# Performance work log

Hardware: AMD Instinct MI355X
Metric: run time of the kernel (lower is better)

## Reference

```python
import jax, jax.numpy as jnp
import numpy as np

NOISE_DIM = 32
HIDDEN_DIM = 256
DATA_DIM = 2
TEMP = 0.05
N = 16384
DIAG_PENALTY = 1e6


def _cdist(a, b):
    # Euclidean pairwise distance [Na, Nb], safe sqrt (zero grad at d==0 like torch.cdist)
    d2 = (jnp.sum(a * a, -1)[:, None] + jnp.sum(b * b, -1)[None, :]
          - 2.0 * (a @ b.T))
    d2 = jnp.maximum(d2, 0.0)
    safe = jnp.where(d2 > 0, d2, 1.0)
    return jnp.where(d2 > 0, jnp.sqrt(safe), 0.0)


def setup_inputs() -> dict:
    key = jax.random.key(0)
    ks = jax.random.split(key, 12)
    pos = jax.random.normal(ks[0], (N, DATA_DIM), dtype=jnp.float32)
    z = jax.random.normal(ks[1], (N, NOISE_DIM), dtype=jnp.float32)
    def lin(k, fan_in, fan_out):
        bound = 1.0 / np.sqrt(fan_in)
        k1, k2 = jax.random.split(k)
        W = jax.random.uniform(k1, (fan_in, fan_out), minval=-bound, maxval=bound, dtype=jnp.float32)
        b = jax.random.uniform(k2, (fan_out,), minval=-bound, maxval=bound, dtype=jnp.float32)
        return W, b
    W1, b1 = lin(ks[2], NOISE_DIM, HIDDEN_DIM)
    W2, b2 = lin(ks[3], HIDDEN_DIM, HIDDEN_DIM)
    W3, b3 = lin(ks[4], HIDDEN_DIM, HIDDEN_DIM)
    W4, b4 = lin(ks[5], HIDDEN_DIM, HIDDEN_DIM)
    W5, b5 = lin(ks[6], HIDDEN_DIM, DATA_DIM)
    return {"pos": pos, "z": z, "W1": W1, "b1": b1, "W2": W2, "b2": b2,
            "W3": W3, "b3": b3, "W4": W4, "b4": b4, "W5": W5, "b5": b5}


def reference(pos, z, W1, b1, W2, b2, W3, b3, W4, b4, W5, b5):
    # SELU MLP generator
    h = jax.nn.selu(z @ W1 + b1)
    h = jax.nn.selu(h @ W2 + b2)
    h = jax.nn.selu(h @ W3 + b3)
    h = jax.nn.selu(h @ W4 + b4)
    gen = h @ W5 + b5  # [N, D]

    y_pos = jax.lax.stop_gradient(pos)
    y_neg = jax.lax.stop_gradient(gen)

    dist_pos = _cdist(gen, y_pos)  # [N, N]
    dist_neg = _cdist(gen, y_neg)  # [N, N]
    dist_neg = dist_neg + jnp.eye(gen.shape[0], dtype=gen.dtype) * DIAG_PENALTY

    energy_pos = -TEMP * jax.nn.logsumexp(-dist_pos / TEMP, axis=1)
    energy_neg = TEMP * jax.nn.logsumexp(-dist_neg / TEMP, axis=1)
    return energy_pos + energy_neg  # [N]
```

## Files before the change

kernel.cpp:

```cpp
#include <hip/hip_runtime.h>
#include <hip/hip_bf16.h>

#define N_PTS 16384
#define TEMP_F 0.05f

typedef __attribute__((ext_vector_type(8))) short bf16x8;
typedef __attribute__((ext_vector_type(4))) float f32x4;

__device__ __forceinline__ float selu_f(float x) {
    const float scale = 1.0507009873554805f;
    const float alpha = 1.6732632423543772f;
    return x > 0.f ? scale * x : scale * alpha * (__expf(x) - 1.f);
}

__device__ __forceinline__ float fast_sqrtf(float x) {
#if __has_builtin(__builtin_amdgcn_sqrtf)
    return __builtin_amdgcn_sqrtf(x);
#else
    return sqrtf(x);
#endif
}

__device__ __forceinline__ float fast_exp2f(float x) {
#if __has_builtin(__builtin_amdgcn_exp2f)
    return __builtin_amdgcn_exp2f(x);
#else
    return exp2f(x);
#endif
}

__device__ __forceinline__ float fast_log2f(float x) {
#if __has_builtin(__builtin_amdgcn_logf)
    return __builtin_amdgcn_logf(x);
#else
    return log2f(x);
#endif
}

__device__ __forceinline__ f32x4 mfma_bf16(bf16x8 a, bf16x8 b, f32x4 c) {
    return __builtin_amdgcn_mfma_f32_16x16x32_bf16(a, b, c, 0, 0, 0);
}

__device__ __forceinline__ void split_bf16(float v, unsigned short& hi, unsigned short& lo) {
    unsigned u = __float_as_uint(v);
    hi = (unsigned short)(u >> 16);
    float ah = __uint_as_float(u & 0xFFFF0000u);
    lo = (unsigned short)(__float_as_uint(v - ah) >> 16);
}

__global__ __launch_bounds__(256) void pack_kernel(
    const float* __restrict__ W1, const float* __restrict__ W2,
    const float* __restrict__ W3, const float* __restrict__ W4,
    unsigned short* __restrict__ pk)
{
    int idx = blockIdx.x * 256 + threadIdx.x;
    if (idx >= 25600) return;
    const float* src;
    unsigned short *dh, *dl;
    int nt, kc, l, KC;
    if (idx < 1024) {
        src = W1; dh = pk; dl = pk + 8192; KC = 1;
        nt = idx >> 6; kc = 0; l = idx & 63;
    } else {
        int t2 = idx - 1024;
        int ly = t2 >> 13;
        int r2 = t2 & 8191;
        src = (ly == 0) ? W2 : (ly == 1) ? W3 : W4;
        dh = pk + 16384 + ly * 131072;
        dl = dh + 65536;
        KC = 8;
        nt = r2 >> 9; kc = (r2 >> 6) & 7; l = r2 & 63;
    }
    int lr = l & 15, lq = l >> 4;
    int n = nt * 16 + lr;
    bf16x8 hv, lv;
    #pragma unroll
    for (int e = 0; e < 8; e++) {
        int k = kc * 32 + lq * 8 + e;
        float v = src[k * 256 + n];
        unsigned short hb, lb;
        split_bf16(v, hb, lb);
        hv[e] = (short)hb; lv[e] = (short)lb;
    }
    int base = ((nt * KC + kc) * 64 + l) * 8;
    *(bf16x8*)(dh + base) = hv;
    *(bf16x8*)(dl + base) = lv;
}

__global__ __launch_bounds__(512) void mlp_mfma_kernel(
    const float* __restrict__ z,
    const unsigned short* __restrict__ pk,
    const float* __restrict__ b1, const float* __restrict__ b2,
    const float* __restrict__ b3, const float* __restrict__ b4,
    const float* __restrict__ W5, const float* __restrict__ b5,
    float* __restrict__ gen)
{
    __shared__ __align__(16) unsigned short Hh[32 * 256];
    __shared__ __align__(16) unsigned short Hl[32 * 256];

    const int t  = threadIdx.x;
    const int l  = t & 63;
    const int wv = t >> 6;
    const int lr = l & 15;
    const int lq = l >> 4;
    const int row0 = blockIdx.x * 32;

    f32x4 acc[2][2];

    {
        bf16x8 ah[2], al[2];
        #pragma unroll
        for (int m = 0; m < 2; m++) {
            const float* zp = z + (row0 + m * 16 + lr) * 32 + lq * 8;
            f32x4 z0 = *(const f32x4*)(zp);
            f32x4 z1 = *(const f32x4*)(zp + 4);
            #pragma unroll
            for (int e = 0; e < 8; e++) {
                float v = (e < 4) ? z0[e] : z1[e - 4];
                unsigned short hb, lb;
                split_bf16(v, hb, lb);
                ah[m][e] = (short)hb; al[m][e] = (short)lb;
            }
        }
        #pragma unroll
        for (int n2 = 0; n2 < 2; n2++) {
            float bv = b1[wv * 32 + n2 * 16 + lr];
            #pragma unroll
            for (int m = 0; m < 2; m++) acc[m][n2] = (f32x4){bv, bv, bv, bv};
        }
        const bf16x8* B1h = (const bf16x8*)(pk);
        const bf16x8* B1l = (const bf16x8*)(pk + 8192);
        #pragma unroll
        for (int n2 = 0; n2 < 2; n2++) {
            int nt = wv * 2 + n2;
            bf16x8 bh = B1h[nt * 64 + l];
            bf16x8 bl = B1l[nt * 64 + l];
            #pragma unroll
            for (int m = 0; m < 2; m++) {
                acc[m][n2] = mfma_bf16(ah[m], bh, acc[m][n2]);
                acc[m][n2] = mfma_bf16(ah[m], bl, acc[m][n2]);
                acc[m][n2] = mfma_bf16(al[m], bh, acc[m][n2]);
            }
        }
        #pragma unroll
        for (int m = 0; m < 2; m++) {
            #pragma unroll
            for (int n2 = 0; n2 < 2; n2++) {
                #pragma unroll
                for (int r = 0; r < 4; r++) {
                    float v = selu_f(acc[m][n2][r]);
                    int rowo = m * 16 + lq * 4 + r;
                    int n = wv * 32 + n2 * 16 + lr;
                    int o = (2 * n) ^ ((rowo & 7) << 4);
                    unsigned short hb, lb;
                    split_bf16(v, hb, lb);
                    Hh[rowo * 256 + (o >> 1)] = hb;
                    Hl[rowo * 256 + (o >> 1)] = lb;
                }
            }
        }
    }
    __syncthreads();

    #pragma unroll 1
    for (int ly = 0; ly < 3; ly++) {
        const unsigned short* wbase = pk + 16384 + ly * 131072;
        const bf16x8* Bh = (const bf16x8*)(wbase);
        const bf16x8* Bl = (const bf16x8*)(wbase + 65536);
        const float* bb = (ly == 0) ? b2 : (ly == 1) ? b3 : b4;
        #pragma unroll
        for (int n2 = 0; n2 < 2; n2++) {
            float bv = bb[wv * 32 + n2 * 16 + lr];
            #pragma unroll
            for (int m = 0; m < 2; m++) acc[m][n2] = (f32x4){bv, bv, bv, bv};
        }
        #pragma unroll 4
        for (int kc = 0; kc < 8; kc++) {
            bf16x8 ah[2], al[2];
            #pragma unroll
            for (int m = 0; m < 2; m++) {
                int arow = m * 16 + lr;
                int o = (kc * 64 + lq * 16) ^ ((arow & 7) << 4);
                ah[m] = *(const bf16x8*)(Hh + arow * 256 + (o >> 1));
                al[m] = *(const bf16x8*)(Hl + arow * 256 + (o >> 1));
            }
            #pragma unroll
            for (int n2 = 0; n2 < 2; n2++) {
                bf16x8 bh = Bh[((wv * 2 + n2) * 8 + kc) * 64 + l];
                bf16x8 bl = Bl[((wv * 2 + n2) * 8 + kc) * 64 + l];
                #pragma unroll
                for (int m = 0; m < 2; m++) {
                    acc[m][n2] = mfma_bf16(ah[m], bh, acc[m][n2]);
                    acc[m][n2] = mfma_bf16(ah[m], bl, acc[m][n2]);
                    acc[m][n2] = mfma_bf16(al[m], bh, acc[m][n2]);
                }
            }
        }
        __syncthreads();
        #pragma unroll
        for (int m = 0; m < 2; m++) {
            #pragma unroll
            for (int n2 = 0; n2 < 2; n2++) {
                #pragma unroll
                for (int r = 0; r < 4; r++) {
                    float v = selu_f(acc[m][n2][r]);
                    int rowo = m * 16 + lq * 4 + r;
                    int n = wv * 32 + n2 * 16 + lr;
                    int o = (2 * n) ^ ((rowo & 7) << 4);
                    unsigned short hb, lb;
                    split_bf16(v, hb, lb);
                    Hh[rowo * 256 + (o >> 1)] = hb;
                    Hl[rowo * 256 + (o >> 1)] = lb;
                }
            }
        }
        __syncthreads();
    }

    if (t < 64) {
        int row = t & 31;
        int d = t >> 5;
        float sum = b5[d];
        #pragma unroll 4
        for (int k = 0; k < 256; k += 8) {
            int o = (2 * k) ^ ((row & 7) << 4);
            bf16x8 hh = *(const bf16x8*)(Hh + row * 256 + (o >> 1));
            bf16x8 ll = *(const bf16x8*)(Hl + row * 256 + (o >> 1));
            #pragma unroll
            for (int e = 0; e < 8; e++) {
                float hv = __uint_as_float(((unsigned)(unsigned short)hh[e]) << 16)
                         + __uint_as_float(((unsigned)(unsigned short)ll[e]) << 16);
                sum = fmaf(hv, W5[(k + e) * 2 + d], sum);
            }
        }
        gen[(row0 + row) * 2 + d] = sum;
    }
}

__global__ __launch_bounds__(1024) void mlp_kernel(
    const float* __restrict__ z,
    const float* __restrict__ W1, const float* __restrict__ b1,
    const float* __restrict__ W2, const float* __restrict__ b2,
    const float* __restrict__ W3, const float* __restrict__ b3,
    const float* __restrict__ W4, const float* __restrict__ b4,
    const float* __restrict__ W5, const float* __restrict__ b5,
    float* __restrict__ gen)
{
    __shared__ float h[256 * 64];

    const int t = threadIdx.x;
    const int r = t & 63;
    const int w = __builtin_amdgcn_readfirstlane(t >> 6);
    const int c0 = w * 16;
    const int row0 = blockIdx.x * 64;

    #pragma unroll
    for (int e = 0; e < 2; e++) {
        int f  = t + e * 1024;
        int rz = f >> 5;
        int kz = f & 31;
        h[kz * 64 + rz] = z[(row0 + rz) * 32 + kz];
    }
    __syncthreads();

    float acc[16];

    #pragma unroll
    for (int j = 0; j < 16; j++) acc[j] = b1[c0 + j];
    #pragma unroll 8
    for (int k = 0; k < 32; k++) {
        float hv = h[k * 64 + r];
        const float* Wr = W1 + k * 256 + c0;
        #pragma unroll
        for (int j = 0; j < 16; j++) acc[j] = fmaf(hv, Wr[j], acc[j]);
    }
    __syncthreads();
    #pragma unroll
    for (int j = 0; j < 16; j++) h[(c0 + j) * 64 + r] = selu_f(acc[j]);
    __syncthreads();

    for (int layer = 0; layer < 3; layer++) {
        const float* W = (layer == 0) ? W2 : (layer == 1) ? W3 : W4;
        const float* b = (layer == 0) ? b2 : (layer == 1) ? b3 : b4;
        #pragma unroll
        for (int j = 0; j < 16; j++) acc[j] = b[c0 + j];
        #pragma unroll 4
        for (int k = 0; k < 256; k++) {
            float hv = h[k * 64 + r];
            const float* Wr = W + k * 256 + c0;
            #pragma unroll
            for (int j = 0; j < 16; j++) acc[j] = fmaf(hv, Wr[j], acc[j]);
        }
        __syncthreads();
        #pragma unroll
        for (int j = 0; j < 16; j++) h[(c0 + j) * 64 + r] = selu_f(acc[j]);
        __syncthreads();
    }

    float p0 = 0.f, p1 = 0.f;
    #pragma unroll
    for (int kk = 0; kk < 16; kk++) {
        int k = c0 + kk;
        float hv = h[k * 64 + r];
        p0 = fmaf(hv, W5[k * 2 + 0], p0);
        p1 = fmaf(hv, W5[k * 2 + 1], p1);
    }
    __syncthreads();
    h[(0 * 16 + w) * 64 + r] = p0;
    h[(1 * 16 + w) * 64 + r] = p1;
    __syncthreads();
    if (t < 128) {
        int d  = t >> 6;
        int rr = t & 63;
        float sum = b5[d];
        #pragma unroll
        for (int ss = 0; ss < 16; ss++) sum += h[(d * 16 + ss) * 64 + rr];
        gen[(row0 + rr) * 2 + d] = sum;
    }
}

__global__ __launch_bounds__(512) void energy_kernel(
    const float* __restrict__ gen,
    const float* __restrict__ pos,
    float* __restrict__ out,
    int row_off)
{
    __shared__ float4 sp[512];
    __shared__ float4 sg[512];

    const int t  = threadIdx.x;
    const int s  = t & 31;
    const int rl = t >> 5;
    const int i  = row_off + blockIdx.x * 16 + rl;
    const int diagBase = ((row_off + blockIdx.x * 16) >> 10) << 10;

    const float2 q = ((const float2*)gen)[i];

    const float cL2 = 28.853900817779268f;
    const float Tl2 = 0.034657359027997264f;
    const float cB  = 57.707801635558536f;

    float p0 = 0.f, p1 = 0.f, n0 = 0.f, n1 = 0.f;

    for (int base = 0; base < N_PTS; base += 1024) {
        __syncthreads();
        sp[t] = ((const float4*)pos)[base / 2 + t];
        sg[t] = ((const float4*)gen)[base / 2 + t];
        __syncthreads();
        if (base == diagBase) {
            #pragma unroll 4
            for (int u = 0; u < 16; u++) {
                int j = base + 2 * (s + 32 * u);
                float4 pp = sp[s + 32 * u];
                float4 gg = sg[s + 32 * u];
                float dx = q.x - pp.x, dy = q.y - pp.y;
                float d  = fast_sqrtf(fmaf(dx, dx, dy * dy));
                p0 += fast_exp2f(fmaf(-cL2, d, cB));
                dx = q.x - pp.z; dy = q.y - pp.w;
                d  = fast_sqrtf(fmaf(dx, dx, dy * dy));
                p1 += fast_exp2f(fmaf(-cL2, d, cB));
                dx = q.x - gg.x; dy = q.y - gg.y;
                d  = fast_sqrtf(fmaf(dx, dx, dy * dy));
                float e0 = fast_exp2f(fmaf(-cL2, d, cB));
                n0 += (j == i) ? 0.f : e0;
                dx = q.x - gg.z; dy = q.y - gg.w;
                d  = fast_sqrtf(fmaf(dx, dx, dy * dy));
                float e1 = fast_exp2f(fmaf(-cL2, d, cB));
                n1 += (j + 1 == i) ? 0.f : e1;
            }
        } else {
            #pragma unroll 4
            for (int u = 0; u < 16; u++) {
                float4 pp = sp[s + 32 * u];
                float4 gg = sg[s + 32 * u];
                float dx = q.x - pp.x, dy = q.y - pp.y;
                float d  = fast_sqrtf(fmaf(dx, dx, dy * dy));
                p0 += fast_exp2f(fmaf(-cL2, d, cB));
                dx = q.x - pp.z; dy = q.y - pp.w;
                d  = fast_sqrtf(fmaf(dx, dx, dy * dy));
                p1 += fast_exp2f(fmaf(-cL2, d, cB));
                dx = q.x - gg.x; dy = q.y - gg.y;
                d  = fast_sqrtf(fmaf(dx, dx, dy * dy));
                n0 += fast_exp2f(fmaf(-cL2, d, cB));
                dx = q.x - gg.z; dy = q.y - gg.w;
                d  = fast_sqrtf(fmaf(dx, dx, dy * dy));
                n1 += fast_exp2f(fmaf(-cL2, d, cB));
            }
        }
    }

    float sump = p0 + p1;
    float sumn = n0 + n1;
    #pragma unroll
    for (int m = 1; m < 32; m <<= 1) {
        sump += __shfl_xor(sump, m, 32);
        sumn += __shfl_xor(sumn, m, 32);
    }

    if (s == 0) {
        out[i] = Tl2 * (fast_log2f(sumn) - fast_log2f(sump));
    }
}

extern "C" void kernel_launch(void* const* d_in, const int* in_sizes, int n_in,
                              void* d_out, int out_size, void* d_ws, size_t ws_size,
                              hipStream_t stream) {
    const float* pos = (const float*)d_in[0];
    const float* z   = (const float*)d_in[1];
    const float* W1  = (const float*)d_in[2];
    const float* b1  = (const float*)d_in[3];
    const float* W2  = (const float*)d_in[4];
    const float* b2  = (const float*)d_in[5];
    const float* W3  = (const float*)d_in[6];
    const float* b3  = (const float*)d_in[7];
    const float* W4  = (const float*)d_in[8];
    const float* b4  = (const float*)d_in[9];
    const float* W5  = (const float*)d_in[10];
    const float* b5  = (const float*)d_in[11];

    float* gen = (float*)d_ws;
    unsigned short* pk = (unsigned short*)((char*)d_ws + 131072);
    const size_t WS_NEEDED = 131072 + (size_t)409600 * 2;

    if (ws_size >= WS_NEEDED) {
        pack_kernel<<<100, 256, 0, stream>>>(W1, W2, W3, W4, pk);
        mlp_mfma_kernel<<<N_PTS / 32, 512, 0, stream>>>(z, pk, b1, b2, b3, b4,
                                                        W5, b5, gen);
    } else {
        mlp_kernel<<<N_PTS / 64, 1024, 0, stream>>>(z, W1, b1, W2, b2, W3, b3,
                                                    W4, b4, W5, b5, gen);
    }
    energy_kernel<<<N_PTS / 32, 512, 0, stream>>>(gen, pos, (float*)d_out, 0);
    energy_kernel<<<N_PTS / 32, 512, 0, stream>>>(gen, pos, (float*)d_out, 8192);
}
```

Measured before the change: 249.0 us.

## Fuse weight packing, MLP and energy into one cooperative kernel

Replaces the four separate launches (pack, MLP, two energy halves) with a single cooperative kernel of 512 blocks that uses grid-wide syncs between the weight-packing, MLP and pairwise-energy phases. Each block handles 32 MLP rows and then 2x16 energy rows. The intent is to remove launch overhead and the gaps between kernels. In exchange it adds grid-sync costs, requires all 512 blocks of 512 threads to be co-resident, and runs the energy phase with each block striding across both halves. The fallback path also changes the energy launch grid to N/16 blocks with a row offset of 0.

```diff
diff --git a/kernel.cpp b/kernel.cpp
--- a/kernel.cpp
+++ b/kernel.cpp
@@ -1,5 +1,8 @@
 #include <hip/hip_runtime.h>
 #include <hip/hip_bf16.h>
+#include <hip/hip_cooperative_groups.h>
+
+namespace cg = cooperative_groups;
 
 #define N_PTS 16384
 #define TEMP_F 0.05f
@@ -47,6 +50,277 @@
     float ah = __uint_as_float(u & 0xFFFF0000u);
     lo = (unsigned short)(__float_as_uint(v - ah) >> 16);
 }
+
+__global__ __launch_bounds__(512, 4) void fused_kernel(
+    const float* pos, const float* z,
+    const float* W1, const float* b1, const float* W2, const float* b2,
+    const float* W3, const float* b3, const float* W4, const float* b4,
+    const float* W5, const float* b5,
+    unsigned short* pk, float* gen, float* out)
+{
+    __shared__ __align__(16) unsigned short Hh[32 * 256];
+    __shared__ __align__(16) unsigned short Hl[32 * 256];
+    __shared__ float4 sp[512];
+    __shared__ float4 sg[512];
+
+    const int t = threadIdx.x;
+
+    if (blockIdx.x < 50) {
+        int idx = blockIdx.x * 512 + t;
+        const float* src;
+        unsigned short *dh, *dl;
+        int nt, kc, lx, KC;
+        if (idx < 1024) {
+            src = W1; dh = pk; dl = pk + 8192; KC = 1;
+            nt = idx >> 6; kc = 0; lx = idx & 63;
+        } else {
+            int t2 = idx - 1024;
+            int ly = t2 >> 13;
+            int r2 = t2 & 8191;
+            src = (ly == 0) ? W2 : (ly == 1) ? W3 : W4;
+            dh = pk + 16384 + ly * 131072;
+            dl = dh + 65536;
+            KC = 8;
+            nt = r2 >> 9; kc = (r2 >> 6) & 7; lx = r2 & 63;
+        }
+        int lrp = lx & 15, lqp = lx >> 4;
+        int n = nt * 16 + lrp;
+        bf16x8 hv, lv;
+        #pragma unroll
+        for (int e = 0; e < 8; e++) {
+            int k = kc * 32 + lqp * 8 + e;
+            float v = src[k * 256 + n];
+            unsigned short hb, lb;
+            split_bf16(v, hb, lb);
+            hv[e] = (short)hb; lv[e] = (short)lb;
+        }
+        int basep = ((nt * KC + kc) * 64 + lx) * 8;
+        *(bf16x8*)(dh + basep) = hv;
+        *(bf16x8*)(dl + basep) = lv;
+    }
+    __threadfence();
+    cg::this_grid().sync();
+
+    {
+        const int l  = t & 63;
+        const int wv = t >> 6;
+        const int lr = l & 15;
+        const int lq = l >> 4;
+        const int row0 = blockIdx.x * 32;
+
+        f32x4 acc[2][2];
+
+        {
+            bf16x8 ah[2], al[2];
+            #pragma unroll
+            for (int m = 0; m < 2; m++) {
+                const float* zp = z + (row0 + m * 16 + lr) * 32 + lq * 8;
+                f32x4 z0 = *(const f32x4*)(zp);
+                f32x4 z1 = *(const f32x4*)(zp + 4);
+                #pragma unroll
+                for (int e = 0; e < 8; e++) {
+                    float v = (e < 4) ? z0[e] : z1[e - 4];
+                    unsigned short hb, lb;
+                    split_bf16(v, hb, lb);
+                    ah[m][e] = (short)hb; al[m][e] = (short)lb;
+                }
+            }
+            #pragma unroll
+            for (int n2 = 0; n2 < 2; n2++) {
+                float bv = b1[wv * 32 + n2 * 16 + lr];
+                #pragma unroll
+                for (int m = 0; m < 2; m++) acc[m][n2] = (f32x4){bv, bv, bv, bv};
+            }
+            const bf16x8* B1h = (const bf16x8*)(pk);
+            const bf16x8* B1l = (const bf16x8*)(pk + 8192);
+            #pragma unroll
+            for (int n2 = 0; n2 < 2; n2++) {
+                int nt = wv * 2 + n2;
+                bf16x8 bh = B1h[nt * 64 + l];
+                bf16x8 bl = B1l[nt * 64 + l];
+                #pragma unroll
+                for (int m = 0; m < 2; m++) {
+                    acc[m][n2] = mfma_bf16(ah[m], bh, acc[m][n2]);
+                    acc[m][n2] = mfma_bf16(ah[m], bl, acc[m][n2]);
+                    acc[m][n2] = mfma_bf16(al[m], bh, acc[m][n2]);
+                }
+            }
+            #pragma unroll
+            for (int m = 0; m < 2; m++) {
+                #pragma unroll
+                for (int n2 = 0; n2 < 2; n2++) {
+                    #pragma unroll
+                    for (int r = 0; r < 4; r++) {
+                        float v = selu_f(acc[m][n2][r]);
+                        int rowo = m * 16 + lq * 4 + r;
+                        int n = wv * 32 + n2 * 16 + lr;
+                        int o = (2 * n) ^ ((rowo & 7) << 4);
+                        unsigned short hb, lb;
+                        split_bf16(v, hb, lb);
+                        Hh[rowo * 256 + (o >> 1)] = hb;
+                        Hl[rowo * 256 + (o >> 1)] = lb;
+                    }
+                }
+            }
+        }
+        __syncthreads();
+
+        #pragma unroll 1
+        for (int ly = 0; ly < 3; ly++) {
+            const unsigned short* wbase = pk + 16384 + ly * 131072;
+            const bf16x8* Bh = (const bf16x8*)(wbase);
+            const bf16x8* Bl = (const bf16x8*)(wbase + 65536);
+            const float* bb = (ly == 0) ? b2 : (ly == 1) ? b3 : b4;
+            #pragma unroll
+            for (int n2 = 0; n2 < 2; n2++) {
+                float bv = bb[wv * 32 + n2 * 16 + lr];
+                #pragma unroll
+                for (int m = 0; m < 2; m++) acc[m][n2] = (f32x4){bv, bv, bv, bv};
+            }
+            #pragma unroll 4
+            for (int kc = 0; kc < 8; kc++) {
+                bf16x8 ah[2], al[2];
+                #pragma unroll
+                for (int m = 0; m < 2; m++) {
+                    int arow = m * 16 + lr;
+                    int o = (kc * 64 + lq * 16) ^ ((arow & 7) << 4);
+                    ah[m] = *(const bf16x8*)(Hh + arow * 256 + (o >> 1));
+                    al[m] = *(const bf16x8*)(Hl + arow * 256 + (o >> 1));
+                }
+                #pragma unroll
+                for (int n2 = 0; n2 < 2; n2++) {
+                    bf16x8 bh = Bh[((wv * 2 + n2) * 8 + kc) * 64 + l];
+                    bf16x8 bl = Bl[((wv * 2 + n2) * 8 + kc) * 64 + l];
+                    #pragma unroll
+                    for (int m = 0; m < 2; m++) {
+                        acc[m][n2] = mfma_bf16(ah[m], bh, acc[m][n2]);
+                        acc[m][n2] = mfma_bf16(ah[m], bl, acc[m][n2]);
+                        acc[m][n2] = mfma_bf16(al[m], bh, acc[m][n2]);
+                    }
+                }
+            }
+            __syncthreads();
+            #pragma unroll
+            for (int m = 0; m < 2; m++) {
+                #pragma unroll
+                for (int n2 = 0; n2 < 2; n2++) {
+                    #pragma unroll
+                    for (int r = 0; r < 4; r++) {
+                        float v = selu_f(acc[m][n2][r]);
+                        int rowo = m * 16 + lq * 4 + r;
+                        int n = wv * 32 + n2 * 16 + lr;
+                        int o = (2 * n) ^ ((rowo & 7) << 4);
+                        unsigned short hb, lb;
+                        split_bf16(v, hb, lb);
+                        Hh[rowo * 256 + (o >> 1)] = hb;
+                        Hl[rowo * 256 + (o >> 1)] = lb;
+                    }
+                }
+            }
+            __syncthreads();
+        }
+
+        if (t < 64) {
+            int row = t & 31;
+            int d = t >> 5;
+            float sum = b5[d];
+            #pragma unroll 4
+            for (int k = 0; k < 256; k += 8) {
+                int o = (2 * k) ^ ((row & 7) << 4);
+                bf16x8 hh = *(const bf16x8*)(Hh + row * 256 + (o >> 1));
+                bf16x8 ll = *(const bf16x8*)(Hl + row * 256 + (o >> 1));
+                #pragma unroll
+                for (int e = 0; e < 8; e++) {
+                    float hv = __uint_as_float(((unsigned)(unsigned short)hh[e]) << 16)
+                             + __uint_as_float(((unsigned)(unsigned short)ll[e]) << 16);
+                    sum = fmaf(hv, W5[(k + e) * 2 + d], sum);
+                }
+            }
+            gen[(row0 + row) * 2 + d] = sum;
+        }
+    }
+    __threadfence();
+    cg::this_grid().sync();
+
+    {
+        const int s  = t & 31;
+        const int rl = t >> 5;
+
+        const float cL2 = 28.853900817779268f;
+        const float Tl2 = 0.034657359027997264f;
+        const float cB  = 57.707801635558536f;
+
+        #pragma unroll 1
+        for (int c = 0; c < 2; c++) {
+            const int row_off = c * 8192;
+            const int i = row_off + blockIdx.x * 16 + rl;
+            const int diagBase = ((row_off + blockIdx.x * 16) >> 10) << 10;
+
+            const float2 q = ((const float2*)gen)[i];
+            float p0 = 0.f, p1 = 0.f, n0 = 0.f, n1 = 0.f;
+
+            for (int base = 0; base < N_PTS; base += 1024) {
+                __syncthreads();
+                sp[t] = ((const float4*)pos)[base / 2 + t];
+                sg[t] = ((const float4*)gen)[base / 2 + t];
+                __syncthreads();
+                if (base == diagBase) {
+                    #pragma unroll 4
+                    for (int u = 0; u < 16; u++) {
+                        int j = base + 2 * (s + 32 * u);
+                        float4 pp = sp[s + 32 * u];
+                        float4 gg = sg[s + 32 * u];
+                        float dx = q.x - pp.x, dy = q.y - pp.y;
+                        float d  = fast_sqrtf(fmaf(dx, dx, dy * dy));
+                        p0 += fast_exp2f(fmaf(-cL2, d, cB));
+                        dx = q.x - pp.z; dy = q.y - pp.w;
+                        d  = fast_sqrtf(fmaf(dx, dx, dy * dy));
+                        p1 += fast_exp2f(fmaf(-cL2, d, cB));
+                        dx = q.x - gg.x; dy = q.y - gg.y;
+                        d  = fast_sqrtf(fmaf(dx, dx, dy * dy));
+                        float e0 = fast_exp2f(fmaf(-cL2, d, cB));
+                        n0 += (j == i) ? 0.f : e0;
+                        dx = q.x - gg.z; dy = q.y - gg.w;
+                        d  = fast_sqrtf(fmaf(dx, dx, dy * dy));
+                        float e1 = fast_exp2f(fmaf(-cL2, d, cB));
+                        n1 += (j + 1 == i) ? 0.f : e1;
+                    }
+                } else {
+                    #pragma unroll 4
+                    for (int u = 0; u < 16; u++) {
+                        float4 pp = sp[s + 32 * u];
+                        float4 gg = sg[s + 32 * u];
+                        float dx = q.x - pp.x, dy = q.y - pp.y;
+                        float d  = fast_sqrtf(fmaf(dx, dx, dy * dy));
+                        p0 += fast_exp2f(fmaf(-cL2, d, cB));
+                        dx = q.x - pp.z; dy = q.y - pp.w;
+                        d  = fast_sqrtf(fmaf(dx, dx, dy * dy));
+                        p1 += fast_exp2f(fmaf(-cL2, d, cB));
+                        dx = q.x - gg.x; dy = q.y - gg.y;
+                        d  = fast_sqrtf(fmaf(dx, dx, dy * dy));
+                        n0 += fast_exp2f(fmaf(-cL2, d, cB));
+                        dx = q.x - gg.z; dy = q.y - gg.w;
+                        d  = fast_sqrtf(fmaf(dx, dx, dy * dy));
+                        n1 += fast_exp2f(fmaf(-cL2, d, cB));
+                    }
+                }
+            }
+
+            float sump = p0 + p1;
+            float sumn = n0 + n1;
+            #pragma unroll
+            for (int m = 1; m < 32; m <<= 1) {
+                sump += __shfl_xor(sump, m, 32);
+                sumn += __shfl_xor(sumn, m, 32);
+            }
+            if (s == 0) {
+                out[i] = Tl2 * (fast_log2f(sumn) - fast_log2f(sump));
+            }
+            __syncthreads();
+        }
+    }
+}
+
 
 __global__ __launch_bounds__(256) void pack_kernel(
     const float* __restrict__ W1, const float* __restrict__ W2,
@@ -420,16 +694,28 @@
 
     float* gen = (float*)d_ws;
     unsigned short* pk = (unsigned short*)((char*)d_ws + 131072);
+    float* outp = (float*)d_out;
     const size_t WS_NEEDED = 131072 + (size_t)409600 * 2;
 
     if (ws_size >= WS_NEEDED) {
+        void* args[] = {
+            (void*)&pos, (void*)&z,
+            (void*)&W1, (void*)&b1, (void*)&W2, (void*)&b2,
+            (void*)&W3, (void*)&b3, (void*)&W4, (void*)&b4,
+            (void*)&W5, (void*)&b5,
+            (void*)&pk, (void*)&gen, (void*)&outp
+        };
+        hipError_t err = hipLaunchCooperativeKernel(
+            reinterpret_cast<void*>(fused_kernel),
+            dim3(512), dim3(512), args, 0, stream);
+        if (err == hipSuccess) return;
         pack_kernel<<<100, 256, 0, stream>>>(W1, W2, W3, W4, pk);
         mlp_mfma_kernel<<<N_PTS / 32, 512, 0, stream>>>(z, pk, b1, b2, b3, b4,
                                                         W5, b5, gen);
+        energy_kernel<<<N_PTS / 16, 512, 0, stream>>>(gen, pos, outp, 0);
     } else {
         mlp_kernel<<<N_PTS / 64, 1024, 0, stream>>>(z, W1, b1, W2, b2, W3, b3,
                                                     W4, b4, W5, b5, gen);
-    }
-    energy_kernel<<<N_PTS / 32, 512, 0, stream>>>(gen, pos, (float*)d_out, 0);
-    energy_kernel<<<N_PTS / 32, 512, 0, stream>>>(gen, pos, (float*)d_out, 8192);
-}
+        energy_kernel<<<N_PTS / 16, 512, 0, stream>>>(gen, pos, outp, 0);
+    }
+}
```

New measurement: 514.2 us. 2.07x slower.
